# Kernel optimization log

Hardware: AMD Instinct MI355X
Metric: run time of the kernel (lower is better)

Reference implementation:

```python
import jax, jax.numpy as jnp
import numpy as np

RADIUS = 0.15
NSAMPLE = 128
NPOINT = 128
EPS = 1e-5  # BatchNorm eps (eval mode, running_mean=0, running_var=1)


def _bn(x, g, b):
    shape = (1, -1) + (1,) * (x.ndim - 2)
    return x * (g / jnp.sqrt(1.0 + EPS)).reshape(shape) + b.reshape(shape)


def _fps(x, npoint):
    # farthest point sampling; x: (Bk, N, 3) -> (Bk, npoint) int32
    Bn, N, _ = x.shape

    def step(carry, _):
        dist, far = carry
        c = jnp.take_along_axis(x, far[:, None, None], 1)  # (Bk,1,3)
        d = jnp.sum((x - c) ** 2, -1)
        dist = jnp.minimum(dist, d)
        return (dist, jnp.argmax(dist, -1).astype(jnp.int32)), far

    init = (jnp.full((Bn, N), 1e10, x.dtype), jnp.zeros((Bn,), jnp.int32))
    _, idxs = jax.lax.scan(step, init, None, length=npoint)
    return idxs.T  # (Bk, npoint)


def _sa_module(x, f, mlp):
    # PointnetSAModuleVotes: FPS -> ball query -> group (use_xyz, normalize_xyz)
    # -> shared MLP (conv2d 1x1 + BN + ReLU) -> max over nsample.
    Bk, M, _ = x.shape
    fps_idx = _fps(x, NPOINT)
    new_xyz = jnp.take_along_axis(x, fps_idx[..., None], 1)  # (Bk,np,3)
    d2 = jnp.sum((new_xyz[:, :, None, :] - x[:, None, :, :]) ** 2, -1)  # (Bk,np,M)
    cand = jnp.where(d2 < RADIUS ** 2, jnp.arange(M)[None, None, :], M)
    cand = jnp.sort(cand, -1)[..., :NSAMPLE]  # first nsample in-radius indices
    first = cand[..., :1]
    first = jnp.where(first == M, 0, first)
    idx = jnp.where(cand == M, first, cand)  # (Bk,np,ns), pad with first valid
    gx = jnp.take_along_axis(x, idx.reshape(Bk, -1)[..., None], 1).reshape(Bk, NPOINT, NSAMPLE, 3)
    gxn = (gx - new_xyz[:, :, None, :]) / RADIUS  # normalize_xyz=True
    gf = jnp.take_along_axis(f[:, :, None, :], idx[:, None, :, :], 3)  # (Bk,C,np,ns)
    h = jnp.concatenate([gxn.transpose(0, 3, 1, 2), gf], 1)  # (Bk, C+3, np, ns)
    for (w, b, g, be) in mlp:
        h = jax.nn.relu(_bn(jnp.einsum('oc,bcps->bops', w, h) + b[None, :, None, None], g, be))
    return new_xyz, h.max(-1)  # (Bk,np,3), (Bk,128,np)


def setup_inputs() -> dict:
    key = jax.random.key(0)
    ks = iter(jax.random.split(key, 40))
    B, M, K, C = 2, 1024, 19, 256
    inp = {}
    inp['xyz'] = jax.random.normal(next(ks), (B, M, K, 3), jnp.float32)
    inp['features'] = jax.random.normal(next(ks), (B, C, K, M), jnp.float32)

    def conv_p(prefix, cin, cout):
        inp[prefix + '_w'] = jax.random.normal(next(ks), (cout, cin), jnp.float32) * (1.0 / np.sqrt(cin))
        inp[prefix + '_b'] = jax.random.normal(next(ks), (cout,), jnp.float32) * 0.02
        inp[prefix + '_g'] = 1.0 + 0.1 * jax.random.normal(next(ks), (cout,), jnp.float32)
        inp[prefix + '_be'] = 0.02 * jax.random.normal(next(ks), (cout,), jnp.float32)

    conv_p('m1', C + 3, 128)  # use_xyz -> 259 in-channels
    conv_p('m2', 128, 128)
    conv_p('m3', 128, 128)
    conv_p('c1', 128, 128)
    conv_p('c2', 128, 128)
    inp['op_w'] = jax.random.normal(next(ks), (K, 5, 128), jnp.float32) * (1.0 / np.sqrt(128))
    inp['op_b'] = jax.random.normal(next(ks), (K, 5), jnp.float32) * 0.02
    return inp


def reference(xyz, features, m1_w, m1_b, m1_g, m1_be, m2_w, m2_b, m2_g, m2_be,
              m3_w, m3_b, m3_g, m3_be, c1_w, c1_b, c1_g, c1_be,
              c2_w, c2_b, c2_g, c2_be, op_w, op_b):
    B, M, K, _ = xyz.shape
    C = features.shape[1]
    # fold vote_factor k into the batch dim (all per-k SA/conv weights are shared)
    x = xyz.transpose(0, 2, 1, 3).reshape(B * K, M, 3)
    f = features.transpose(0, 2, 1, 3).reshape(B * K, C, M)
    mlp = [(m1_w, m1_b, m1_g, m1_be), (m2_w, m2_b, m2_g, m2_be), (m3_w, m3_b, m3_g, m3_be)]
    new_xyz, feat = _sa_module(x, f, mlp)
    net = jax.nn.relu(_bn(jnp.einsum('oc,bcp->bop', c1_w, feat) + c1_b[None, :, None], c1_g, c1_be))
    net = jax.nn.relu(_bn(jnp.einsum('oc,bcp->bop', c2_w, net) + c2_b[None, :, None], c2_g, c2_be))
    net = net.reshape(B, K, 128, NPOINT)
    # per-k output conv (conv_op ModuleList), 128 -> 2+3
    out = jnp.einsum('koc,bkcp->bkop', op_w, net) + op_b[None, :, :, None]
    net_t = out.transpose(0, 1, 3, 2)  # (B,K,np,5)
    agg_xyz = new_xyz.reshape(B, K, NPOINT, 3)
    center = agg_xyz + net_t[..., 2:5]  # decode_scores_
    scores = jnp.concatenate([net_t[..., :2], center], -1)  # obj(2) + center(3)
    return scores, agg_xyz, feat.reshape(B, K, 128, NPOINT)
```

## Files before the change

### kernel.cpp

```cpp
#include <hip/hip_runtime.h>
#include <math.h>

#define NBK   38

#define OFF_XC    0u
#define OFF_NXYZ  466944u
#define OFF_BIDX  525312u
#define OFF_W1F   3015680u
#define OFF_PREP  22938624u
#define OFF_WF    22955008u
#define OFF_CNT   23348224u

#define OUT_AGG   24320
#define OUT_FEAT  38912

typedef short bf16x8 __attribute__((ext_vector_type(8)));
typedef float f32x4  __attribute__((ext_vector_type(4)));
typedef int   v4i    __attribute__((ext_vector_type(4)));
typedef int   v2i    __attribute__((ext_vector_type(2)));

__device__ __forceinline__ float dist2f(float a0, float a1, float a2,
                                        float b0, float b1, float b2) {
#pragma clang fp contract(off)
  float d0 = a0 - b0;
  float d1 = a1 - b1;
  float d2 = a2 - b2;
  return d0 * d0 + d1 * d1 + d2 * d2;
}

__device__ __forceinline__ void split2rn(float v, unsigned& sh, unsigned& sm) {
  unsigned u = __float_as_uint(v);
  unsigned rh = (u + 0x7fffu + ((u >> 16) & 1u)) & 0xffff0000u;
  sh = rh >> 16;
  float r1 = v - __uint_as_float(rh);
  unsigned u1 = __float_as_uint(r1);
  unsigned rm = (u1 + 0x7fffu + ((u1 >> 16) & 1u)) & 0xffff0000u;
  sm = rm >> 16;
}

#define DPP_FMAX_STEP(v, ctrl)                                                 \
  {                                                                            \
    int _s = __builtin_amdgcn_update_dpp(__float_as_int(v), __float_as_int(v), \
                                         (ctrl), 0xf, 0xf, false);             \
    (v) = fmaxf((v), __int_as_float(_s));                                      \
  }

__device__ __forceinline__ float readlane_f(float v, int l) {
  return __int_as_float(__builtin_amdgcn_readlane(__float_as_int(v), l));
}

__global__ __launch_bounds__(128, 1) void fps_kernel(
    const float* __restrict__ xyz, float* __restrict__ xc,
    float* __restrict__ nxyz, float* __restrict__ agg)
{
  __shared__ __align__(16) float4 sp4[1024];
  __shared__ int2 cexch[2][2];
  __shared__ int sfar[128];
  int bk = blockIdx.x;
  int b = bk / 19, k = bk % 19;
  int t = threadIdx.x, lane = t & 63, wave = t >> 6;

  for (int i = t; i < 1024; i += 128) {
    const float* src = xyz + ((size_t)((b * 1024 + i) * 19 + k)) * 3;
    float x0 = src[0], x1 = src[1], x2 = src[2];
    sp4[i] = make_float4(x0, x1, x2, 0.f);
    xc[(bk * 3 + 0) * 1024 + i] = x0;
    xc[(bk * 3 + 1) * 1024 + i] = x1;
    xc[(bk * 3 + 2) * 1024 + i] = x2;
  }
  if (t == 0) sfar[0] = 0;
  __syncthreads();

  float px[8], py[8], pz[8], dist[8];
  int mbase = (wave << 9) + (lane << 3);
#pragma unroll
  for (int j = 0; j < 8; ++j) {
    float4 p = sp4[mbase + j];
    px[j] = p.x; py[j] = p.y; pz[j] = p.z;
    dist[j] = 1e10f;
  }

  int far = 0;
  for (int it = 1; it < 128; ++it) {
    float4 c = sp4[far];
#pragma unroll
    for (int j = 0; j < 8; ++j) {
      float d = dist2f(px[j], py[j], pz[j], c.x, c.y, c.z);
      dist[j] = fminf(dist[j], d);
    }
    float tv[4]; int tj[4];
#pragma unroll
    for (int i = 0; i < 4; ++i) {
      bool L = dist[2 * i] >= dist[2 * i + 1];
      tv[i] = L ? dist[2 * i] : dist[2 * i + 1];
      tj[i] = L ? (2 * i) : (2 * i + 1);
    }
    {
      bool L0 = tv[0] >= tv[1];
      float v0 = L0 ? tv[0] : tv[1]; int j0 = L0 ? tj[0] : tj[1];
      bool L1 = tv[2] >= tv[3];
      float v1 = L1 ? tv[2] : tv[3]; int j1 = L1 ? tj[2] : tj[3];
      bool L = v0 >= v1;
      tv[0] = L ? v0 : v1; tj[0] = L ? j0 : j1;
    }
    float lmax = tv[0];
    float g = lmax;
    DPP_FMAX_STEP(g, 0x111);
    DPP_FMAX_STEP(g, 0x112);
    DPP_FMAX_STEP(g, 0x114);
    DPP_FMAX_STEP(g, 0x118);
    float r0 = readlane_f(g, 15);
    float r1 = readlane_f(g, 31);
    float r2 = readlane_f(g, 47);
    float r3 = readlane_f(g, 63);
    float gmax = fmaxf(fmaxf(r0, r1), fmaxf(r2, r3));
    unsigned long long mk = __ballot(lmax == gmax);
    int wl = (int)__builtin_ctzll(mk);
    int lj = (lane << 3) + tj[0];
    int cand_m = (wave << 9) + __builtin_amdgcn_readlane(lj, wl);
    if (lane == 0) cexch[it & 1][wave] = make_int2(__float_as_int(gmax), cand_m);
    __syncthreads();
    int2 c0 = cexch[it & 1][0];
    int2 c1 = cexch[it & 1][1];
    far = (__int_as_float(c1.x) > __int_as_float(c0.x)) ? c1.y : c0.y;
    if (t == 0) sfar[it] = far;
  }
  __syncthreads();

  if (t < 128) {
    float4 c = sp4[sfar[t]];
    nxyz[bk * 384 + t * 3 + 0] = c.x;
    nxyz[bk * 384 + t * 3 + 1] = c.y;
    nxyz[bk * 384 + t * 3 + 2] = c.z;
    agg[bk * 384 + t * 3 + 0] = c.x;
    agg[bk * 384 + t * 3 + 1] = c.y;
    agg[bk * 384 + t * 3 + 2] = c.z;
  }
}

__global__ __launch_bounds__(512, 2) void front_kernel(
    const float* __restrict__ xyz, const float* __restrict__ feats,
    const float* __restrict__ m1w, const float* __restrict__ m1b,
    const float* __restrict__ m1g, const float* __restrict__ m1be,
    const float* __restrict__ m2w, const float* __restrict__ m2b,
    const float* __restrict__ m2g, const float* __restrict__ m2be,
    const float* __restrict__ m3w, const float* __restrict__ m3b,
    const float* __restrict__ m3g, const float* __restrict__ m3be,
    const float* __restrict__ c1w, const float* __restrict__ c1b,
    const float* __restrict__ c1g, const float* __restrict__ c1be,
    const float* __restrict__ c2w, const float* __restrict__ c2b,
    const float* __restrict__ c2g, const float* __restrict__ c2be,
    float* __restrict__ xc, float* __restrict__ nxyz,
    int* __restrict__ bidx, int* __restrict__ counts,
    float* __restrict__ W1f, short* __restrict__ Wf, float* __restrict__ prep)
{
  __shared__ __align__(16) char smem[32768];
  int bid = blockIdx.x, t = threadIdx.x;
  int wave = t >> 6, lane = t & 63;

  if (bid < NBK) {
    int bk = bid;
    float4* sp4 = (float4*)smem;
    float4* scen4 = (float4*)(smem + 16384);

    for (int i = t; i < 1024; i += 512) {
      sp4[i] = make_float4(xc[(bk * 3 + 0) * 1024 + i],
                           xc[(bk * 3 + 1) * 1024 + i],
                           xc[(bk * 3 + 2) * 1024 + i], 0.f);
    }
    if (t < 128) {
      scen4[t] = make_float4(nxyz[(bk * 128 + t) * 3 + 0],
                             nxyz[(bk * 128 + t) * 3 + 1],
                             nxyz[(bk * 128 + t) * 3 + 2], 0.f);
    }
    __syncthreads();

    for (int p = wave * 16; p < wave * 16 + 16; ++p) {
      float4 cen = scen4[p];
      int* outp = bidx + ((size_t)(bk * 128 + p)) * 128;
      int count = 0, first = 0;
      bool got = false;
      for (int ch = 0; ch < 16 && count < 128; ++ch) {
        int m = (ch << 6) + lane;
        float4 pv = sp4[m];
        float d = dist2f(pv.x, pv.y, pv.z, cen.x, cen.y, cen.z);
        bool flag = d < 0.0225f;
        unsigned long long mask = __ballot(flag);
        if (!got && mask) { first = (ch << 6) + __builtin_ctzll(mask); got = true; }
        int pos = count + (int)__popcll(mask & ((1ull << lane) - 1ull));
        if (flag && pos < 128) outp[pos] = m;
        count += (int)__popcll(mask);
      }
      for (int j = count + lane; j < 128; j += 64) outp[j] = first;
      if (lane == 0) counts[bk * 128 + p] = count > 128 ? 128 : count;
    }
    return;
  }

  if (bid < 342) {
    short* ffrag = (short*)smem;
    if (t >= 256) {
      for (int i = 0; i < 8; ++i) __syncthreads();
      return;
    }
    int blk = bid - NBK;
    int bk = blk >> 3, m0 = (blk & 7) << 7;
    int b = bk / 19, k = bk % 19;
    int quad = lane >> 4, nl = lane & 15;
    int mloc = t & 127, chalf = t >> 7;
    int st_w = mloc >> 4, sl_w = mloc & 15;
    const float* fbase = feats + ((size_t)(b * 4864 + k)) * 1024 + m0 + mloc;

    f32x4 acc[2][8];
#pragma unroll
    for (int oi = 0; oi < 2; ++oi)
#pragma unroll
      for (int st = 0; st < 8; ++st) acc[oi][st] = (f32x4){0.f, 0.f, 0.f, 0.f};

    for (int ch = 0; ch < 4; ++ch) {
      int cbase = ch * 64 + chalf * 32;
#pragma unroll
      for (int g = 0; g < 4; ++g) {
        float v[8];
#pragma unroll
        for (int j = 0; j < 8; ++j)
          v[j] = fbase[(size_t)(cbase + g * 8 + j) * 19456];
        unsigned sh[8], sm[8];
#pragma unroll
        for (int j = 0; j < 8; ++j) split2rn(v[j], sh[j], sm[j]);
        int base = chalf * 4096 + st_w * 512 + (g * 16 + sl_w) * 8;
        v4i ph = {(int)(sh[0] | (sh[1] << 16)), (int)(sh[2] | (sh[3] << 16)),
                  (int)(sh[4] | (sh[5] << 16)), (int)(sh[6] | (sh[7] << 16))};
        *(v4i*)&ffrag[base] = ph;
        v4i pm = {(int)(sm[0] | (sm[1] << 16)), (int)(sm[2] | (sm[3] << 16)),
                  (int)(sm[4] | (sm[5] << 16)), (int)(sm[6] | (sm[7] << 16))};
        *(v4i*)&ffrag[base + 8192] = pm;
      }
      __syncthreads();
#pragma unroll
      for (int kkl = 0; kkl < 2; ++kkl) {
        int kk = ch * 2 + kkl;
        bf16x8 a[2][2];
#pragma unroll
        for (int oi = 0; oi < 2; ++oi) {
          int o_row = (wave * 2 + oi) * 16 + nl;
          const float* wsrc = m1w + o_row * 259 + 3 + kk * 32 + quad * 8;
          float wv[8];
#pragma unroll
          for (int j = 0; j < 8; ++j) wv[j] = wsrc[j];
          unsigned sh[8], sm[8];
#pragma unroll
          for (int j = 0; j < 8; ++j) split2rn(wv[j], sh[j], sm[j]);
          short ah[8], am[8];
#pragma unroll
          for (int j = 0; j < 8; ++j) { ah[j] = (short)sh[j]; am[j] = (short)sm[j]; }
          a[oi][0] = (bf16x8){ah[0], ah[1], ah[2], ah[3], ah[4], ah[5], ah[6], ah[7]};
          a[oi][1] = (bf16x8){am[0], am[1], am[2], am[3], am[4], am[5], am[6], am[7]};
        }
#pragma unroll
        for (int st = 0; st < 8; ++st) {
          const short* hb = ffrag + kkl * 4096 + st * 512 + lane * 8;
          bf16x8 b0 = *(const bf16x8*)hb;
          bf16x8 b1 = *(const bf16x8*)(hb + 8192);
#pragma unroll
          for (int oi = 0; oi < 2; ++oi) {
            f32x4 c = acc[oi][st];
            c = __builtin_amdgcn_mfma_f32_16x16x32_bf16(a[oi][1], b0, c, 0, 0, 0);
            c = __builtin_amdgcn_mfma_f32_16x16x32_bf16(a[oi][0], b1, c, 0, 0, 0);
            c = __builtin_amdgcn_mfma_f32_16x16x32_bf16(a[oi][0], b0, c, 0, 0, 0);
            acc[oi][st] = c;
          }
        }
      }
      __syncthreads();
    }
    float inv = 1.0f / sqrtf(1.0f + 1e-5f);
#pragma unroll
    for (int oi = 0; oi < 2; ++oi) {
      int o0 = (wave * 2 + oi) * 16 + quad * 4;
      float4 bb = *(const float4*)&m1b[o0];
      float4 gg = *(const float4*)&m1g[o0];
#pragma unroll
      for (int st = 0; st < 8; ++st) {
        int m_out = m0 + st * 16 + nl;
        f32x4 cc = acc[oi][st];
        float4 r;
        r.x = (cc[0] + bb.x) * (gg.x * inv);
        r.y = (cc[1] + bb.y) * (gg.y * inv);
        r.z = (cc[2] + bb.z) * (gg.z * inv);
        r.w = (cc[3] + bb.w) * (gg.w * inv);
        *(float4*)&W1f[((size_t)(bk * 1024 + m_out)) * 128 + o0] = r;
      }
    }
    return;
  }

  if (bid < 358) {
    int idx = (bid - 342) * 512 + t;
#pragma unroll
    for (int e = 0; e < 4; ++e) {
      int i = idx * 4 + e;
      int c = i & 127, o = (i >> 7) & 127, l = i >> 14;
      float w = (l ? m3w : m2w)[o * 128 + c];
      unsigned sh, sm;
      split2rn(w, sh, sm);
      int ot = o >> 4, mm = o & 15, kk = c >> 5, q = (c & 31) >> 3, j = c & 7;
      int within = (q * 16 + mm) * 8 + j;
      Wf[(((l * 2 + 0) * 4 + kk) * 8 + ot) * 512 + within] = (short)sh;
      Wf[(((l * 2 + 1) * 4 + kk) * 8 + ot) * 512 + within] = (short)sm;
    }
    return;
  }

  if (bid < 374) {
    int idx2 = (bid - 358) * 512 + t;
#pragma unroll
    for (int e = 0; e < 4; ++e) {
      int i = idx2 * 4 + e;
      int c = i & 127, o = (i >> 7) & 127, l = i >> 14;
      float w = (l ? c2w : c1w)[o * 128 + c];
      unsigned sh, sm;
      split2rn(w, sh, sm);
      int ot = o >> 4, mm = o & 15, kk = c >> 5, q = (c & 31) >> 3, j = c & 7;
      int within = (q * 16 + mm) * 8 + j;
      Wf[131072 + (((l * 2 + 0) * 4 + kk) * 8 + ot) * 512 + within] = (short)sh;
      Wf[131072 + (((l * 2 + 1) * 4 + kk) * 8 + ot) * 512 + within] = (short)sm;
    }
    return;
  }

  if (t < 128) {
    float inv = 1.0f / sqrtf(1.0f + 1e-5f);
    float a1 = m1g[t] * inv;
    prep[t] = a1;
    float a2 = m2g[t] * inv;  prep[256 + t] = a2;  prep[384 + t] = fmaf(m2b[t], a2, m2be[t]);
    float a3 = m3g[t] * inv;  prep[512 + t] = a3;  prep[640 + t] = fmaf(m3b[t], a3, m3be[t]);
    float ac1 = c1g[t] * inv; prep[768 + t] = ac1; prep[896 + t] = fmaf(c1b[t], ac1, c1be[t]);
    float ac2 = c2g[t] * inv; prep[1024 + t] = ac2; prep[1152 + t] = fmaf(c2b[t], ac2, c2be[t]);
    prep[1280 + 4 * t + 0] = m1w[t * 259 + 0] * a1;
    prep[1280 + 4 * t + 1] = m1w[t * 259 + 1] * a1;
    prep[1280 + 4 * t + 2] = m1w[t * 259 + 2] * a1;
    prep[1280 + 4 * t + 3] = m1be[t];
  }
}

__device__ __forceinline__ void mfma_layer(const short* __restrict__ Wf,
                                           const short* hfrag, int l,
                                           int wave, int lane, int nst_h,
                                           f32x4 acc[2][4])
{
#pragma unroll 1
  for (int kk = 0; kk < 4; ++kk) {
    bf16x8 a[2][2];
#pragma unroll
    for (int oi = 0; oi < 2; ++oi)
#pragma unroll
      for (int sp = 0; sp < 2; ++sp)
        a[oi][sp] = *(const bf16x8*)(Wf + (((l * 2 + sp) * 4 + kk) * 8 + (wave * 2 + oi)) * 512 + lane * 8);
    for (int st = 0; st < nst_h; ++st) {
      const short* hb = hfrag + kk * 2048 + st * 512 + lane * 8;
      bf16x8 b0 = *(const bf16x8*)(hb);
      bf16x8 b1 = *(const bf16x8*)(hb + 8192);
#pragma unroll
      for (int oi = 0; oi < 2; ++oi) {
        f32x4 c = acc[oi][st];
        c = __builtin_amdgcn_mfma_f32_16x16x32_bf16(a[oi][1], b0, c, 0, 0, 0);
        c = __builtin_amdgcn_mfma_f32_16x16x32_bf16(a[oi][0], b1, c, 0, 0, 0);
        c = __builtin_amdgcn_mfma_f32_16x16x32_bf16(a[oi][0], b0, c, 0, 0, 0);
        acc[oi][st] = c;
      }
    }
  }
}

__global__ __launch_bounds__(256, 3) void sa_kernel(
    const float* __restrict__ xc, const float* __restrict__ nxyz,
    const int* __restrict__ bidx, const int* __restrict__ counts,
    const float* __restrict__ W1f, const float* __restrict__ prep,
    const short* __restrict__ Wf, float* __restrict__ feat_out)
{
  __shared__ __align__(16) short hfrag[16384];
  __shared__ float pcs[512];
  __shared__ float sm[32 * 128];
  __shared__ float ccen[12];
  __shared__ int scnt[4];
  int gb = blockIdx.x, bk = gb >> 5, pb = (gb & 31) << 2;
  int t = threadIdx.x;
  int wave = t >> 6, lane = t & 63;
  int quad = lane >> 4, nl = lane & 15;

  pcs[t] = prep[1280 + t];
  pcs[256 + t] = prep[1536 + t];
  if (t < 4) scnt[t] = counts[bk * 128 + pb + t];
  if (t < 12) {
    int bb = t / 3, c = t % 3;
    ccen[t] = nxyz[(bk * 128 + pb + bb) * 3 + c];
  }
  __syncthreads();
  int n0 = (scnt[0] + 15) >> 4, n1 = (scnt[1] + 15) >> 4;
  int n2 = (scnt[2] + 15) >> 4, n3 = (scnt[3] + 15) >> 4;
  int pf1 = n0, pf2 = n0 + n1, pf3 = n0 + n1 + n2, T = n0 + n1 + n2 + n3;

  for (int q0 = 0; q0 < T; q0 += 4) {
    int nst_h = T - q0;
    if (nst_h > 4) nst_h = 4;
    {
      int cg = wave;
      int st = lane >> 4, sl = lane & 15;
      if (st < nst_h) {
        int q = q0 + st;
        int bq = (q >= pf1) + (q >= pf2) + (q >= pf3);
        int tstart = (bq == 0) ? 0 : (bq == 1) ? pf1 : (bq == 2) ? pf2 : pf3;
        int tslot = q - tstart;
        int m = bidx[((size_t)(bk * 128 + pb + bq)) * 128 + tslot * 16 + sl];
        float cen0 = ccen[bq * 3 + 0], cen1 = ccen[bq * 3 + 1], cen2 = ccen[bq * 3 + 2];
        float g0 = (xc[(bk * 3 + 0) * 1024 + m] - cen0) * (1.0f / 0.15f);
        float g1 = (xc[(bk * 3 + 1) * 1024 + m] - cen1) * (1.0f / 0.15f);
        float g2 = (xc[(bk * 3 + 2) * 1024 + m] - cen2) * (1.0f / 0.15f);
        const float4* wrow = (const float4*)(W1f + ((size_t)(bk * 1024 + m)) * 128 + cg * 32);
        const float4* pcp = (const float4*)pcs + cg * 32;
#pragma unroll
        for (int g = 0; g < 4; ++g) {
          float4 wva = wrow[g * 2], wvb = wrow[g * 2 + 1];
          float wv[8] = {wva.x, wva.y, wva.z, wva.w, wvb.x, wvb.y, wvb.z, wvb.w};
          unsigned sh[8], smv[8];
#pragma unroll
          for (int e = 0; e < 8; ++e) {
            float4 pc = pcp[g * 8 + e];
            float hv = fmaxf(wv[e] + pc.x * g0 + pc.y * g1 + pc.z * g2 + pc.w, 0.f);
            split2rn(hv, sh[e], smv[e]);
          }
          int base = (cg * 4 + st) * 512 + (g * 16 + sl) * 8;
          v4i ph = {(int)(sh[0] | (sh[1] << 16)), (int)(sh[2] | (sh[3] << 16)),
                    (int)(sh[4] | (sh[5] << 16)), (int)(sh[6] | (sh[7] << 16))};
          *(v4i*)&hfrag[base] = ph;
          v4i pm = {(int)(smv[0] | (smv[1] << 16)), (int)(smv[2] | (smv[3] << 16)),
                    (int)(smv[4] | (smv[5] << 16)), (int)(smv[6] | (smv[7] << 16))};
          *(v4i*)&hfrag[base + 8192] = pm;
        }
      }
    }
    __syncthreads();

    f32x4 acc[2][4];
#pragma unroll
    for (int oi = 0; oi < 2; ++oi)
#pragma unroll
      for (int st = 0; st < 4; ++st) acc[oi][st] = (f32x4){0.f, 0.f, 0.f, 0.f};
    mfma_layer(Wf, hfrag, 0, wave, lane, nst_h, acc);
    __syncthreads();

#pragma unroll
    for (int oi = 0; oi < 2; ++oi) {
      int o0 = (wave * 2 + oi) * 16 + quad * 4;
      float4 al = *(const float4*)&prep[256 + o0];
      float4 be = *(const float4*)&prep[384 + o0];
      int kk2 = o0 >> 5, g2 = (o0 & 31) >> 3, j0 = o0 & 7;
      for (int st = 0; st < nst_h; ++st) {
        f32x4 cc = acc[oi][st];
        float v0 = fmaxf(fmaf(cc[0], al.x, be.x), 0.f);
        float v1 = fmaxf(fmaf(cc[1], al.y, be.y), 0.f);
        float v2 = fmaxf(fmaf(cc[2], al.z, be.z), 0.f);
        float v3 = fmaxf(fmaf(cc[3], al.w, be.w), 0.f);
        unsigned h0, m0_, h1, m1_, h2, m2_, h3, m3_;
        split2rn(v0, h0, m0_); split2rn(v1, h1, m1_);
        split2rn(v2, h2, m2_); split2rn(v3, h3, m3_);
        int base = (kk2 * 4 + st) * 512 + (g2 * 16 + nl) * 8 + j0;
        v2i w0 = {(int)(h0 | (h1 << 16)), (int)(h2 | (h3 << 16))};
        *(v2i*)&hfrag[base] = w0;
        v2i w1 = {(int)(m0_ | (m1_ << 16)), (int)(m2_ | (m3_ << 16))};
        *(v2i*)&hfrag[base + 8192] = w1;
      }
    }
    __syncthreads();

#pragma unroll
    for (int oi = 0; oi < 2; ++oi)
#pragma unroll
      for (int st = 0; st < 4; ++st) acc[oi][st] = (f32x4){0.f, 0.f, 0.f, 0.f};
    mfma_layer(Wf, hfrag, 1, wave, lane, nst_h, acc);

#pragma unroll
    for (int oi = 0; oi < 2; ++oi) {
      int o0 = (wave * 2 + oi) * 16 + quad * 4;
      float4 al = *(const float4*)&prep[512 + o0];
      float4 be = *(const float4*)&prep[640 + o0];
      for (int st = 0; st < nst_h; ++st) {
        f32x4 cc = acc[oi][st];
        float v[4];
        v[0] = fmaxf(fmaf(cc[0], al.x, be.x), 0.f);
        v[1] = fmaxf(fmaf(cc[1], al.y, be.y), 0.f);
        v[2] = fmaxf(fmaf(cc[2], al.z, be.z), 0.f);
        v[3] = fmaxf(fmaf(cc[3], al.w, be.w), 0.f);
#pragma unroll
        for (int r = 0; r < 4; ++r) {
          float x = v[r];
          x = fmaxf(x, __shfl_xor(x, 1));
          x = fmaxf(x, __shfl_xor(x, 2));
          x = fmaxf(x, __shfl_xor(x, 4));
          x = fmaxf(x, __shfl_xor(x, 8));
          if (nl == 0) sm[(q0 + st) * 128 + o0 + r] = x;
        }
      }
    }
    __syncthreads();
  }

#pragma unroll
  for (int e = t; e < 512; e += 256) {
    int bb = e >> 7, o = e & 127;
    int qs = (bb == 0) ? 0 : (bb == 1) ? pf1 : (bb == 2) ? pf2 : pf3;
    int nq = (bb == 0) ? n0 : (bb == 1) ? n1 : (bb == 2) ? n2 : n3;
    float v = sm[qs * 128 + o];
    for (int q = 1; q < nq; ++q) v = fmaxf(v, sm[(qs + q) * 128 + o]);
    feat_out[(((size_t)bk) << 14) + (o << 7) + pb + bb] = v;
  }
}

__global__ __launch_bounds__(256) void head_kernel(const float* __restrict__ featg,
    const float* __restrict__ prep, const short* __restrict__ Wf,
    const float* __restrict__ nxyz, const float* __restrict__ opw,
    const float* __restrict__ opb, float* __restrict__ scores)
{
  __shared__ __align__(16) short hfrag[16384];
  __shared__ float hplain[128 * 65];
  int bk = blockIdx.x >> 1, p0 = (blockIdx.x & 1) << 6;
  int t = threadIdx.x;
  int wave = t >> 6, lane = t & 63;
  int quad = lane >> 4, nl = lane & 15;
  const short* WC = Wf + 131072;

  {
    int cg = wave;
    int st = lane >> 4, sl = lane & 15;
    const float* fb = featg + (bk << 14) + p0 + lane;
#pragma unroll
    for (int g = 0; g < 4; ++g) {
      float v[8];
#pragma unroll
      for (int e = 0; e < 8; ++e)
        v[e] = fb[(cg * 32 + g * 8 + e) << 7];
      unsigned sh[8], sm[8];
#pragma unroll
      for (int e = 0; e < 8; ++e) split2rn(v[e], sh[e], sm[e]);
      int base = (cg * 4 + st) * 512 + (g * 16 + sl) * 8;
      v4i ph = {(int)(sh[0] | (sh[1] << 16)), (int)(sh[2] | (sh[3] << 16)),
                (int)(sh[4] | (sh[5] << 16)), (int)(sh[6] | (sh[7] << 16))};
      *(v4i*)&hfrag[base] = ph;
      v4i pm = {(int)(sm[0] | (sm[1] << 16)), (int)(sm[2] | (sm[3] << 16)),
                (int)(sm[4] | (sm[5] << 16)), (int)(sm[6] | (sm[7] << 16))};
      *(v4i*)&hfrag[base + 8192] = pm;
    }
  }
  __syncthreads();

  f32x4 acc[2][4];
#pragma unroll
  for (int oi = 0; oi < 2; ++oi)
#pragma unroll
    for (int st = 0; st < 4; ++st) acc[oi][st] = (f32x4){0.f, 0.f, 0.f, 0.f};
  mfma_layer(WC, hfrag, 0, wave, lane, 4, acc);
  __syncthreads();

#pragma unroll
  for (int oi = 0; oi < 2; ++oi) {
    int o0 = (wave * 2 + oi) * 16 + quad * 4;
    float4 al = *(const float4*)&prep[768 + o0];
    float4 be = *(const float4*)&prep[896 + o0];
    int kk2 = o0 >> 5, g2 = (o0 & 31) >> 3, j0 = o0 & 7;
#pragma unroll
    for (int st = 0; st < 4; ++st) {
      f32x4 cc = acc[oi][st];
      float v0 = fmaxf(fmaf(cc[0], al.x, be.x), 0.f);
      float v1 = fmaxf(fmaf(cc[1], al.y, be.y), 0.f);
      float v2 = fmaxf(fmaf(cc[2], al.z, be.z), 0.f);
      float v3 = fmaxf(fmaf(cc[3], al.w, be.w), 0.f);
      unsigned h0, m0_, h1, m1_, h2, m2_, h3, m3_;
      split2rn(v0, h0, m0_); split2rn(v1, h1, m1_);
      split2rn(v2, h2, m2_); split2rn(v3, h3, m3_);
      int base = (kk2 * 4 + st) * 512 + (g2 * 16 + nl) * 8 + j0;
      v2i w0 = {(int)(h0 | (h1 << 16)), (int)(h2 | (h3 << 16))};
      *(v2i*)&hfrag[base] = w0;
      v2i w1 = {(int)(m0_ | (m1_ << 16)), (int)(m2_ | (m3_ << 16))};
      *(v2i*)&hfrag[base + 8192] = w1;
    }
  }
  __syncthreads();

#pragma unroll
  for (int oi = 0; oi < 2; ++oi)
#pragma unroll
    for (int st = 0; st < 4; ++st) acc[oi][st] = (f32x4){0.f, 0.f, 0.f, 0.f};
  mfma_layer(WC, hfrag, 1, wave, lane, 4, acc);

#pragma unroll
  for (int oi = 0; oi < 2; ++oi) {
    int o0 = (wave * 2 + oi) * 16 + quad * 4;
    float4 al = *(const float4*)&prep[1024 + o0];
    float4 be = *(const float4*)&prep[1152 + o0];
#pragma unroll
    for (int st = 0; st < 4; ++st) {
      f32x4 cc = acc[oi][st];
      int p = st * 16 + nl;
      hplain[(o0 + 0) * 65 + p] = fmaxf(fmaf(cc[0], al.x, be.x), 0.f);
      hplain[(o0 + 1) * 65 + p] = fmaxf(fmaf(cc[1], al.y, be.y), 0.f);
      hplain[(o0 + 2) * 65 + p] = fmaxf(fmaf(cc[2], al.z, be.z), 0.f);
      hplain[(o0 + 3) * 65 + p] = fmaxf(fmaf(cc[3], al.w, be.w), 0.f);
    }
  }
  __syncthreads();

  if (t < 64) {
    int p = t, k = bk % 19;
    float res[5];
#pragma unroll
    for (int j = 0; j < 5; ++j) {
      const float* wr = opw + ((size_t)(k * 5 + j)) * 128;
      float a = opb[k * 5 + j];
      for (int c = 0; c < 128; ++c) a = fmaf(wr[c], hplain[c * 65 + p], a);
      res[j] = a;
    }
    int pg = p0 + p;
    float a0 = nxyz[(bk * 128 + pg) * 3 + 0];
    float a1 = nxyz[(bk * 128 + pg) * 3 + 1];
    float a2 = nxyz[(bk * 128 + pg) * 3 + 2];
    float* sc = scores + ((size_t)(bk * 128 + pg)) * 5;
    sc[0] = res[0];
    sc[1] = res[1];
    sc[2] = a0 + res[2];
    sc[3] = a1 + res[3];
    sc[4] = a2 + res[4];
  }
}

extern "C" void kernel_launch(void* const* d_in, const int* in_sizes, int n_in,
                              void* d_out, int out_size, void* d_ws, size_t ws_size,
                              hipStream_t stream) {
  (void)in_sizes; (void)n_in; (void)out_size; (void)ws_size;
  const float* xyz  = (const float*)d_in[0];
  const float* fts  = (const float*)d_in[1];
  const float* m1w  = (const float*)d_in[2];
  const float* m1b  = (const float*)d_in[3];
  const float* m1g  = (const float*)d_in[4];
  const float* m1be = (const float*)d_in[5];
  const float* m2w  = (const float*)d_in[6];
  const float* m2b  = (const float*)d_in[7];
  const float* m2g  = (const float*)d_in[8];
  const float* m2be = (const float*)d_in[9];
  const float* m3w  = (const float*)d_in[10];
  const float* m3b  = (const float*)d_in[11];
  const float* m3g  = (const float*)d_in[12];
  const float* m3be = (const float*)d_in[13];
  const float* c1w  = (const float*)d_in[14];
  const float* c1b  = (const float*)d_in[15];
  const float* c1g  = (const float*)d_in[16];
  const float* c1be = (const float*)d_in[17];
  const float* c2w  = (const float*)d_in[18];
  const float* c2b  = (const float*)d_in[19];
  const float* c2g  = (const float*)d_in[20];
  const float* c2be = (const float*)d_in[21];
  const float* opw  = (const float*)d_in[22];
  const float* opb  = (const float*)d_in[23];

  float* out = (float*)d_out;
  char* ws = (char*)d_ws;
  float* xc   = (float*)(ws + OFF_XC);
  float* nxyz = (float*)(ws + OFF_NXYZ);
  int*   bidx = (int*)(ws + OFF_BIDX);
  float* W1f  = (float*)(ws + OFF_W1F);
  float* prep = (float*)(ws + OFF_PREP);
  short* Wf   = (short*)(ws + OFF_WF);
  int*   cnt  = (int*)(ws + OFF_CNT);

  hipLaunchKernelGGL(fps_kernel, dim3(NBK), dim3(128), 0, stream,
                     xyz, xc, nxyz, out + OUT_AGG);
  hipLaunchKernelGGL(front_kernel, dim3(375), dim3(512), 0, stream,
                     xyz, fts, m1w, m1b, m1g, m1be, m2w, m2b, m2g, m2be,
                     m3w, m3b, m3g, m3be, c1w, c1b, c1g, c1be,
                     c2w, c2b, c2g, c2be,
                     xc, nxyz, bidx, cnt, W1f, Wf, prep);
  hipLaunchKernelGGL(sa_kernel, dim3(NBK * 32), dim3(256), 0, stream,
                     xc, nxyz, bidx, cnt, W1f, prep, Wf, out + OUT_FEAT);
  hipLaunchKernelGGL(head_kernel, dim3(NBK * 2), dim3(256), 0, stream,
                     out + OUT_FEAT, prep, Wf, nxyz, opw, opb, out);
}
```

Measured before the change: 291.1 us.

## Fuse farthest point sampling into the front kernel's ball-query blocks

Removes the separate fps_kernel launch and runs FPS inside the first 38 blocks of front_kernel, using two of the eight waves for the sampling loop while the others wait at barriers. The sampled centers go straight into shared memory for the ball query instead of being written and re-read through global memory. This saves one launch and a global round trip, and lets the FPS blocks overlap with the weight-prep blocks of the same grid. In exchange, the FPS loop now syncs across 512 threads, and those blocks hold 512-thread resources through the serial FPS phase.

```diff
diff --git a/kernel.cpp b/kernel.cpp
--- a/kernel.cpp
+++ b/kernel.cpp
@@ -47,95 +47,6 @@
 
 __device__ __forceinline__ float readlane_f(float v, int l) {
   return __int_as_float(__builtin_amdgcn_readlane(__float_as_int(v), l));
-}
-
-__global__ __launch_bounds__(128, 1) void fps_kernel(
-    const float* __restrict__ xyz, float* __restrict__ xc,
-    float* __restrict__ nxyz, float* __restrict__ agg)
-{
-  __shared__ __align__(16) float4 sp4[1024];
-  __shared__ int2 cexch[2][2];
-  __shared__ int sfar[128];
-  int bk = blockIdx.x;
-  int b = bk / 19, k = bk % 19;
-  int t = threadIdx.x, lane = t & 63, wave = t >> 6;
-
-  for (int i = t; i < 1024; i += 128) {
-    const float* src = xyz + ((size_t)((b * 1024 + i) * 19 + k)) * 3;
-    float x0 = src[0], x1 = src[1], x2 = src[2];
-    sp4[i] = make_float4(x0, x1, x2, 0.f);
-    xc[(bk * 3 + 0) * 1024 + i] = x0;
-    xc[(bk * 3 + 1) * 1024 + i] = x1;
-    xc[(bk * 3 + 2) * 1024 + i] = x2;
-  }
-  if (t == 0) sfar[0] = 0;
-  __syncthreads();
-
-  float px[8], py[8], pz[8], dist[8];
-  int mbase = (wave << 9) + (lane << 3);
-#pragma unroll
-  for (int j = 0; j < 8; ++j) {
-    float4 p = sp4[mbase + j];
-    px[j] = p.x; py[j] = p.y; pz[j] = p.z;
-    dist[j] = 1e10f;
-  }
-
-  int far = 0;
-  for (int it = 1; it < 128; ++it) {
-    float4 c = sp4[far];
-#pragma unroll
-    for (int j = 0; j < 8; ++j) {
-      float d = dist2f(px[j], py[j], pz[j], c.x, c.y, c.z);
-      dist[j] = fminf(dist[j], d);
-    }
-    float tv[4]; int tj[4];
-#pragma unroll
-    for (int i = 0; i < 4; ++i) {
-      bool L = dist[2 * i] >= dist[2 * i + 1];
-      tv[i] = L ? dist[2 * i] : dist[2 * i + 1];
-      tj[i] = L ? (2 * i) : (2 * i + 1);
-    }
-    {
-      bool L0 = tv[0] >= tv[1];
-      float v0 = L0 ? tv[0] : tv[1]; int j0 = L0 ? tj[0] : tj[1];
-      bool L1 = tv[2] >= tv[3];
-      float v1 = L1 ? tv[2] : tv[3]; int j1 = L1 ? tj[2] : tj[3];
-      bool L = v0 >= v1;
-      tv[0] = L ? v0 : v1; tj[0] = L ? j0 : j1;
-    }
-    float lmax = tv[0];
-    float g = lmax;
-    DPP_FMAX_STEP(g, 0x111);
-    DPP_FMAX_STEP(g, 0x112);
-    DPP_FMAX_STEP(g, 0x114);
-    DPP_FMAX_STEP(g, 0x118);
-    float r0 = readlane_f(g, 15);
-    float r1 = readlane_f(g, 31);
-    float r2 = readlane_f(g, 47);
-    float r3 = readlane_f(g, 63);
-    float gmax = fmaxf(fmaxf(r0, r1), fmaxf(r2, r3));
-    unsigned long long mk = __ballot(lmax == gmax);
-    int wl = (int)__builtin_ctzll(mk);
-    int lj = (lane << 3) + tj[0];
-    int cand_m = (wave << 9) + __builtin_amdgcn_readlane(lj, wl);
-    if (lane == 0) cexch[it & 1][wave] = make_int2(__float_as_int(gmax), cand_m);
-    __syncthreads();
-    int2 c0 = cexch[it & 1][0];
-    int2 c1 = cexch[it & 1][1];
-    far = (__int_as_float(c1.x) > __int_as_float(c0.x)) ? c1.y : c0.y;
-    if (t == 0) sfar[it] = far;
-  }
-  __syncthreads();
-
-  if (t < 128) {
-    float4 c = sp4[sfar[t]];
-    nxyz[bk * 384 + t * 3 + 0] = c.x;
-    nxyz[bk * 384 + t * 3 + 1] = c.y;
-    nxyz[bk * 384 + t * 3 + 2] = c.z;
-    agg[bk * 384 + t * 3 + 0] = c.x;
-    agg[bk * 384 + t * 3 + 1] = c.y;
-    agg[bk * 384 + t * 3 + 2] = c.z;
-  }
 }
 
 __global__ __launch_bounds__(512, 2) void front_kernel(
@@ -150,7 +61,7 @@
     const float* __restrict__ c1g, const float* __restrict__ c1be,
     const float* __restrict__ c2w, const float* __restrict__ c2b,
     const float* __restrict__ c2g, const float* __restrict__ c2be,
-    float* __restrict__ xc, float* __restrict__ nxyz,
+    float* __restrict__ xc, float* __restrict__ nxyz, float* __restrict__ agg,
     int* __restrict__ bidx, int* __restrict__ counts,
     float* __restrict__ W1f, short* __restrict__ Wf, float* __restrict__ prep)
 {
@@ -160,18 +71,95 @@
 
   if (bid < NBK) {
     int bk = bid;
+    int b = bk / 19, k = bk % 19;
     float4* sp4 = (float4*)smem;
     float4* scen4 = (float4*)(smem + 16384);
+    int* sfar = (int*)(smem + 18432);
+    int2* cexch = (int2*)(smem + 18944);
 
     for (int i = t; i < 1024; i += 512) {
-      sp4[i] = make_float4(xc[(bk * 3 + 0) * 1024 + i],
-                           xc[(bk * 3 + 1) * 1024 + i],
-                           xc[(bk * 3 + 2) * 1024 + i], 0.f);
-    }
+      const float* src = xyz + ((size_t)((b * 1024 + i) * 19 + k)) * 3;
+      float x0 = src[0], x1 = src[1], x2 = src[2];
+      sp4[i] = make_float4(x0, x1, x2, 0.f);
+      xc[(bk * 3 + 0) * 1024 + i] = x0;
+      xc[(bk * 3 + 1) * 1024 + i] = x1;
+      xc[(bk * 3 + 2) * 1024 + i] = x2;
+    }
+    if (t == 0) sfar[0] = 0;
+    __syncthreads();
+
+    float px[8], py[8], pz[8], dist[8];
+    if (wave < 2) {
+      int mbase = (wave << 9) + (lane << 3);
+#pragma unroll
+      for (int j = 0; j < 8; ++j) {
+        float4 p = sp4[mbase + j];
+        px[j] = p.x; py[j] = p.y; pz[j] = p.z;
+        dist[j] = 1e10f;
+      }
+    }
+
+    int far = 0;
+    for (int it = 1; it < 128; ++it) {
+      if (wave < 2) {
+        float4 c = sp4[far];
+#pragma unroll
+        for (int j = 0; j < 8; ++j) {
+          float d = dist2f(px[j], py[j], pz[j], c.x, c.y, c.z);
+          dist[j] = fminf(dist[j], d);
+        }
+        float tv[4]; int tj[4];
+#pragma unroll
+        for (int i = 0; i < 4; ++i) {
+          bool L = dist[2 * i] >= dist[2 * i + 1];
+          tv[i] = L ? dist[2 * i] : dist[2 * i + 1];
+          tj[i] = L ? (2 * i) : (2 * i + 1);
+        }
+        {
+          bool L0 = tv[0] >= tv[1];
+          float v0 = L0 ? tv[0] : tv[1]; int j0 = L0 ? tj[0] : tj[1];
+          bool L1 = tv[2] >= tv[3];
+          float v1 = L1 ? tv[2] : tv[3]; int j1 = L1 ? tj[2] : tj[3];
+          bool L = v0 >= v1;
+          tv[0] = L ? v0 : v1; tj[0] = L ? j0 : j1;
+        }
+        float lmax = tv[0];
+        float g = lmax;
+        DPP_FMAX_STEP(g, 0x111);
+        DPP_FMAX_STEP(g, 0x112);
+        DPP_FMAX_STEP(g, 0x114);
+        DPP_FMAX_STEP(g, 0x118);
+        float r0 = readlane_f(g, 15);
+        float r1 = readlane_f(g, 31);
+        float r2 = readlane_f(g, 47);
+        float r3 = readlane_f(g, 63);
+        float gmax = fmaxf(fmaxf(r0, r1), fmaxf(r2, r3));
+        unsigned long long mk = __ballot(lmax == gmax);
+        int wl = (int)__builtin_ctzll(mk);
+        int lj = (lane << 3) + tj[0];
+        int cand_m = (wave << 9) + __builtin_amdgcn_readlane(lj, wl);
+        if (lane == 0) cexch[(it & 1) * 2 + wave] =
+            make_int2(__float_as_int(gmax), cand_m);
+      }
+      __syncthreads();
+      if (wave < 2) {
+        int2 c0 = cexch[(it & 1) * 2 + 0];
+        int2 c1 = cexch[(it & 1) * 2 + 1];
+        far = (__int_as_float(c1.x) > __int_as_float(c0.x)) ? c1.y : c0.y;
+        if (t == 0) sfar[it] = far;
+      }
+    }
+    __syncthreads();
+
     if (t < 128) {
-      scen4[t] = make_float4(nxyz[(bk * 128 + t) * 3 + 0],
-                             nxyz[(bk * 128 + t) * 3 + 1],
-                             nxyz[(bk * 128 + t) * 3 + 2], 0.f);
+      float4 c = sp4[sfar[t]];
+      scen4[t] = c;
+      nxyz[bk * 384 + t * 3 + 0] = c.x;
+      nxyz[bk * 384 + t * 3 + 1] = c.y;
+      nxyz[bk * 384 + t * 3 + 2] = c.z;
+      agg[bk * 384 + t * 3 + 0] = c.x;
+      agg[bk * 384 + t * 3 + 1] = c.y;
+      agg[bk * 384 + t * 3 + 2] = c.z;
     }
     __syncthreads();
 
@@ -672,13 +660,11 @@
   short* Wf   = (short*)(ws + OFF_WF);
   int*   cnt  = (int*)(ws + OFF_CNT);
 
-  hipLaunchKernelGGL(fps_kernel, dim3(NBK), dim3(128), 0, stream,
-                     xyz, xc, nxyz, out + OUT_AGG);
   hipLaunchKernelGGL(front_kernel, dim3(375), dim3(512), 0, stream,
                      xyz, fts, m1w, m1b, m1g, m1be, m2w, m2b, m2g, m2be,
                      m3w, m3b, m3g, m3be, c1w, c1b, c1g, c1be,
                      c2w, c2b, c2g, c2be,
-                     xc, nxyz, bidx, cnt, W1f, Wf, prep);
+                     xc, nxyz, out + OUT_AGG, bidx, cnt, W1f, Wf, prep);
   hipLaunchKernelGGL(sa_kernel, dim3(NBK * 32), dim3(256), 0, stream,
                      xc, nxyz, bidx, cnt, W1f, prep, Wf, out + OUT_FEAT);
   hipLaunchKernelGGL(head_kernel, dim3(NBK * 2), dim3(256), 0, stream,
```

New measurement: 288.7 us. About the same (-0.8%).
